# Optimization experiments

Hardware: AMD Instinct MI355X
Metric: run time of the kernel (lower is better)

The kernel has to match this reference:

```python
import jax, jax.numpy as jnp
import numpy as np

B, N, D_IN, D_OUT = 8, 256, 128, 128
EPS = 1e-5


def setup_inputs() -> dict:
    key = jax.random.key(0)
    ks = jax.random.split(key, 12)
    node_feats = jax.random.normal(ks[0], (B, N, D_IN), dtype=jnp.float32)
    adj_mask = jax.random.randint(ks[1], (B, N, N), 0, 2, dtype=jnp.int32)
    # ensure no fully-masked row (self-loop), matching typical adjacency
    adj_mask = adj_mask.at[:, jnp.arange(N), jnp.arange(N)].set(1)
    rel_positions = jax.random.normal(ks[2], (B, N, N, 2), dtype=jnp.float32)
    s_in = 1.0 / np.sqrt(D_IN)
    s_e = 1.0 / np.sqrt(2 * D_IN + 3)
    s_out = 1.0 / np.sqrt(D_OUT)
    return {
        "node_feats": node_feats,
        "adj_mask": adj_mask,
        "rel_positions": rel_positions,
        "Wn": jax.random.uniform(ks[3], (D_IN, D_OUT), jnp.float32, -s_in, s_in),
        "bn": jax.random.uniform(ks[4], (D_OUT,), jnp.float32, -s_in, s_in),
        "We1": jax.random.uniform(ks[5], (2 * D_IN + 3, D_OUT), jnp.float32, -s_e, s_e),
        "be1": jax.random.uniform(ks[6], (D_OUT,), jnp.float32, -s_e, s_e),
        "We2": jax.random.uniform(ks[7], (D_OUT, 1), jnp.float32, -s_out, s_out),
        "be2": jax.random.uniform(ks[8], (1,), jnp.float32, -s_out, s_out),
        "Wa": jax.random.uniform(ks[9], (D_OUT, D_OUT), jnp.float32, -s_out, s_out),
        "ba": jax.random.uniform(ks[10], (D_OUT,), jnp.float32, -s_out, s_out),
        "gamma": jnp.ones((D_OUT,), jnp.float32),
        "beta": jnp.zeros((D_OUT,), jnp.float32),
    }


def reference(node_feats, adj_mask, rel_positions, Wn, bn, We1, be1, We2, be2, Wa, ba, gamma, beta):
    D = node_feats.shape[-1]
    h = node_feats @ Wn + bn                                # (B,N,Dout)
    # Edge MLP first layer, factored to avoid the (B,N,N,2D+3) concat:
    # edge_input = [h_i, h_j, rel, dist]; Linear(edge_input) splits by rows of We1.
    a_i = node_feats @ We1[:D]                              # source-node part  (B,N,Dout)
    a_j = node_feats @ We1[D:2 * D]                         # target-node part  (B,N,Dout)
    rel_dist = jnp.linalg.norm(rel_positions, axis=-1, keepdims=True)  # (B,N,N,1)
    rel_feat = jnp.concatenate([rel_positions, rel_dist], axis=-1)     # (B,N,N,3)
    a_rel = rel_feat @ We1[2 * D:]                          # (B,N,N,Dout)
    hidden = jax.nn.relu(a_i[:, :, None, :] + a_j[:, None, :, :] + a_rel + be1)
    edge_scores = (hidden @ We2 + be2)[..., 0]              # (B,N,N)
    edge_scores = jnp.where(adj_mask == 0, -jnp.inf, edge_scores)
    w = jax.nn.softmax(edge_scores, axis=-1)
    w = jnp.where(jnp.isnan(w), 0.0, w)                     # fully-masked rows -> 0
    messages = jnp.einsum("bij,bjd->bid", w, h)             # (B,N,Dout)
    aggregated = jax.nn.relu(messages @ Wa + ba)            # dropout in eval mode -> identity
    x = node_feats + aggregated                             # D_IN == D_OUT -> residual
    mu = jnp.mean(x, axis=-1, keepdims=True)
    var = jnp.mean((x - mu) ** 2, axis=-1, keepdims=True)
    return (x - mu) / jnp.sqrt(var + EPS) * gamma + beta
```

## Files before the change

### kernel.cpp

```cpp
#include <hip/hip_runtime.h>
#include <math.h>

#define BB 8
#define NN 256
#define DD 128

#define PR 4
__global__ __launch_bounds__(256) void prep_kernel(
    const float* __restrict__ node, const float* __restrict__ Wn,
    const float* __restrict__ bn, const float* __restrict__ We1,
    const float* __restrict__ be1, float* __restrict__ h,
    float* __restrict__ ti, float* __restrict__ aj)
{
    __shared__ __align__(16) float sx[PR * DD];
    __shared__ float s_acc[12 * 128];
    int tid = threadIdx.x;
    int cp = tid & 63;
    int rp = (tid >> 6) & 1;
    int ks = tid >> 7;
    int row0 = blockIdx.x * PR;
    if (tid < 128) {
        int rr = tid >> 5, cc = (tid & 31) << 2;
        *(float4*)&sx[rr * DD + cc] = *(const float4*)&node[(size_t)(row0 + rr) * DD + cc];
    }
    __syncthreads();
    int d0 = cp << 1;
    int ra = rp << 1, rb = ra | 1;
    float ah[2] = {0.f, 0.f}, ai[2] = {0.f, 0.f}, ajc[2] = {0.f, 0.f};
    float bh[2] = {0.f, 0.f}, bi[2] = {0.f, 0.f}, bjc[2] = {0.f, 0.f};
    int k0 = ks << 6;
    for (int k = k0; k < k0 + 64; k += 4) {
        float4 xa = *(const float4*)&sx[ra * DD + k];
        float4 xb = *(const float4*)&sx[rb * DD + k];
        #pragma unroll
        for (int kk = 0; kk < 4; ++kk) {
            float2 w0 = *(const float2*)&Wn [(size_t)(k + kk) * DD + d0];
            float2 w1 = *(const float2*)&We1[(size_t)(k + kk) * DD + d0];
            float2 w2 = *(const float2*)&We1[(size_t)(DD + k + kk) * DD + d0];
            float xav = (kk == 0) ? xa.x : (kk == 1) ? xa.y : (kk == 2) ? xa.z : xa.w;
            float xbv = (kk == 0) ? xb.x : (kk == 1) ? xb.y : (kk == 2) ? xb.z : xb.w;
            ah[0] = fmaf(xav, w0.x, ah[0]); ah[1] = fmaf(xav, w0.y, ah[1]);
            ai[0] = fmaf(xav, w1.x, ai[0]); ai[1] = fmaf(xav, w1.y, ai[1]);
            ajc[0] = fmaf(xav, w2.x, ajc[0]); ajc[1] = fmaf(xav, w2.y, ajc[1]);
            bh[0] = fmaf(xbv, w0.x, bh[0]); bh[1] = fmaf(xbv, w0.y, bh[1]);
            bi[0] = fmaf(xbv, w1.x, bi[0]); bi[1] = fmaf(xbv, w1.y, bi[1]);
            bjc[0] = fmaf(xbv, w2.x, bjc[0]); bjc[1] = fmaf(xbv, w2.y, bjc[1]);
        }
    }
    int p = (rp << 6) | cp;
    if (ks == 1) {
        s_acc[0 * 128 + p] = ah[0];  s_acc[1 * 128 + p] = ah[1];
        s_acc[2 * 128 + p] = ai[0];  s_acc[3 * 128 + p] = ai[1];
        s_acc[4 * 128 + p] = ajc[0]; s_acc[5 * 128 + p] = ajc[1];
        s_acc[6 * 128 + p] = bh[0];  s_acc[7 * 128 + p] = bh[1];
        s_acc[8 * 128 + p] = bi[0];  s_acc[9 * 128 + p] = bi[1];
        s_acc[10 * 128 + p] = bjc[0]; s_acc[11 * 128 + p] = bjc[1];
    }
    __syncthreads();
    if (ks == 0) {
        float2 bn2  = *(const float2*)&bn[d0];
        float2 be12 = *(const float2*)&be1[d0];
        ah[0] += s_acc[0 * 128 + p] + bn2.x;  ah[1] += s_acc[1 * 128 + p] + bn2.y;
        ai[0] += s_acc[2 * 128 + p] + be12.x; ai[1] += s_acc[3 * 128 + p] + be12.y;
        ajc[0] += s_acc[4 * 128 + p];         ajc[1] += s_acc[5 * 128 + p];
        bh[0] += s_acc[6 * 128 + p] + bn2.x;  bh[1] += s_acc[7 * 128 + p] + bn2.y;
        bi[0] += s_acc[8 * 128 + p] + be12.x; bi[1] += s_acc[9 * 128 + p] + be12.y;
        bjc[0] += s_acc[10 * 128 + p];        bjc[1] += s_acc[11 * 128 + p];
        size_t oa = (size_t)(row0 + ra) * DD + d0;
        size_t ob = (size_t)(row0 + rb) * DD + d0;
        *(float2*)&h [oa] = make_float2(ah[0], ah[1]);
        *(float2*)&ti[oa] = make_float2(ai[0], ai[1]);
        *(float2*)&aj[oa] = make_float2(ajc[0], ajc[1]);
        *(float2*)&h [ob] = make_float2(bh[0], bh[1]);
        *(float2*)&ti[ob] = make_float2(bi[0], bi[1]);
        *(float2*)&aj[ob] = make_float2(bjc[0], bjc[1]);
    }
}

#define IT 4
__global__ __launch_bounds__(256, 2) void edge_kernel(
    const float* __restrict__ ti, const float* __restrict__ ajp,
    const float* __restrict__ rel, const int* __restrict__ adj,
    const float* __restrict__ We1, const float* __restrict__ We2,
    const float* __restrict__ be2, const float* __restrict__ h,
    const float* __restrict__ Wa, const float* __restrict__ ba,
    const float* __restrict__ node, const float* __restrict__ gamma,
    const float* __restrict__ beta, float* __restrict__ out)
{
    __shared__ __align__(16) float s_buf[NN * 32];
    __shared__ __align__(16) float s_w[NN * 4];
    __shared__ __align__(16) float s_m[DD * 4];
    __shared__ float s_red[IT][4];
    __shared__ float s_red2[IT][2][2];

    int tid = threadIdx.x;
    int b  = blockIdx.x >> 6;
    int i0 = (blockIdx.x & 63) << 2;
    int j = tid;

    const float2* rel2 = (const float2*)rel;
    float rx[IT], ry[IT], dsv[IT], sc[IT];
    int msk[IT];
    float be2v = be2[0];
    #pragma unroll
    for (int r = 0; r < IT; ++r) {
        float2 rp = rel2[(size_t)(b * NN + i0 + r) * NN + j];
        rx[r] = rp.x; ry[r] = rp.y;
        dsv[r] = sqrtf(rp.x * rp.x + rp.y * rp.y);
        msk[r] = adj[(size_t)(b * NN + i0 + r) * NN + j];
        sc[r] = be2v;
    }
    const float* TI = ti + (size_t)(b * NN + i0) * DD;
    const float* W0 = We1 + (size_t)(2 * DD + 0) * DD;
    const float* W1 = We1 + (size_t)(2 * DD + 1) * DD;
    const float* W2 = We1 + (size_t)(2 * DD + 2) * DD;
    const float* AJb = ajp + (size_t)b * NN * DD;

    for (int dc = 0; dc < DD; dc += 32) {
        __syncthreads();
        #pragma unroll
        for (int it = 0; it < 8; ++it) {
            int idx = tid + it * 256;
            int rr = idx >> 3, g = idx & 7;
            float4 v = *(const float4*)&AJb[(size_t)rr * DD + dc + (g << 2)];
            *(float4*)&s_buf[rr * 32 + ((g ^ (rr & 7)) << 2)] = v;
        }
        __syncthreads();
        #pragma unroll
        for (int g = 0; g < 8; ++g) {
            float4 a = *(const float4*)&s_buf[j * 32 + ((g ^ (j & 7)) << 2)];
            int dd = dc + (g << 2);
            float4 w0 = *(const float4*)&W0[dd];
            float4 w1 = *(const float4*)&W1[dd];
            float4 w2 = *(const float4*)&W2[dd];
            float4 e2 = *(const float4*)&We2[dd];
            #pragma unroll
            for (int r = 0; r < IT; ++r) {
                float4 t = *(const float4*)&TI[r * DD + dd];
                float v;
                v = fmaf(rx[r], w0.x, t.x + a.x); v = fmaf(ry[r], w1.x, v); v = fmaf(dsv[r], w2.x, v);
                sc[r] = fmaf(fmaxf(v, 0.f), e2.x, sc[r]);
                v = fmaf(rx[r], w0.y, t.y + a.y); v = fmaf(ry[r], w1.y, v); v = fmaf(dsv[r], w2.y, v);
                sc[r] = fmaf(fmaxf(v, 0.f), e2.y, sc[r]);
                v = fmaf(rx[r], w0.z, t.z + a.z); v = fmaf(ry[r], w1.z, v); v = fmaf(dsv[r], w2.z, v);
                sc[r] = fmaf(fmaxf(v, 0.f), e2.z, sc[r]);
                v = fmaf(rx[r], w0.w, t.w + a.w); v = fmaf(ry[r], w1.w, v); v = fmaf(dsv[r], w2.w, v);
                sc[r] = fmaf(fmaxf(v, 0.f), e2.w, sc[r]);
            }
        }
    }
    #pragma unroll
    for (int r = 0; r < IT; ++r) if (msk[r] == 0) sc[r] = -3.0e38f;

    int wave = tid >> 6, lane = tid & 63;
    float e[IT];
    {
        float m[IT];
        #pragma unroll
        for (int r = 0; r < IT; ++r) m[r] = sc[r];
        for (int off = 32; off > 0; off >>= 1) {
            #pragma unroll
            for (int r = 0; r < IT; ++r) m[r] = fmaxf(m[r], __shfl_xor(m[r], off));
        }
        if (lane == 0) {
            #pragma unroll
            for (int r = 0; r < IT; ++r) s_red[r][wave] = m[r];
        }
    }
    __syncthreads();
    #pragma unroll
    for (int r = 0; r < IT; ++r) {
        float M = fmaxf(fmaxf(s_red[r][0], s_red[r][1]), fmaxf(s_red[r][2], s_red[r][3]));
        e[r] = (msk[r] == 0) ? 0.f : __expf(sc[r] - M);
    }
    __syncthreads();
    {
        float s[IT];
        #pragma unroll
        for (int r = 0; r < IT; ++r) s[r] = e[r];
        for (int off = 32; off > 0; off >>= 1) {
            #pragma unroll
            for (int r = 0; r < IT; ++r) s[r] += __shfl_xor(s[r], off);
        }
        if (lane == 0) {
            #pragma unroll
            for (int r = 0; r < IT; ++r) s_red[r][wave] = s[r];
        }
    }
    __syncthreads();
    {
        float4 wq;
        float S0 = s_red[0][0] + s_red[0][1] + s_red[0][2] + s_red[0][3];
        float S1 = s_red[1][0] + s_red[1][1] + s_red[1][2] + s_red[1][3];
        float S2 = s_red[2][0] + s_red[2][1] + s_red[2][2] + s_red[2][3];
        float S3 = s_red[3][0] + s_red[3][1] + s_red[3][2] + s_red[3][3];
        wq.x = e[0] * __builtin_amdgcn_rcpf(S0);
        wq.y = e[1] * __builtin_amdgcn_rcpf(S1);
        wq.z = e[2] * __builtin_amdgcn_rcpf(S2);
        wq.w = e[3] * __builtin_amdgcn_rcpf(S3);
        *(float4*)&s_w[j << 2] = wq;
    }
    __syncthreads();

    float* s_part = s_buf;
    int g3 = tid & 31, sl = tid >> 5;
    {
        const float* hb = h + (size_t)b * NN * DD;
        float4 acc[IT];
        #pragma unroll
        for (int r = 0; r < IT; ++r) acc[r] = make_float4(0.f, 0.f, 0.f, 0.f);
        for (int q = 0; q < 32; ++q) {
            int jj = (sl << 5) + q;
            float4 hv = *(const float4*)&hb[(size_t)jj * DD + (g3 << 2)];
            float4 wv = *(const float4*)&s_w[jj << 2];
            acc[0].x = fmaf(wv.x, hv.x, acc[0].x); acc[0].y = fmaf(wv.x, hv.y, acc[0].y);
            acc[0].z = fmaf(wv.x, hv.z, acc[0].z); acc[0].w = fmaf(wv.x, hv.w, acc[0].w);
            acc[1].x = fmaf(wv.y, hv.x, acc[1].x); acc[1].y = fmaf(wv.y, hv.y, acc[1].y);
            acc[1].z = fmaf(wv.y, hv.z, acc[1].z); acc[1].w = fmaf(wv.y, hv.w, acc[1].w);
            acc[2].x = fmaf(wv.z, hv.x, acc[2].x); acc[2].y = fmaf(wv.z, hv.y, acc[2].y);
            acc[2].z = fmaf(wv.z, hv.z, acc[2].z); acc[2].w = fmaf(wv.z, hv.w, acc[2].w);
            acc[3].x = fmaf(wv.w, hv.x, acc[3].x); acc[3].y = fmaf(wv.w, hv.y, acc[3].y);
            acc[3].z = fmaf(wv.w, hv.z, acc[3].z); acc[3].w = fmaf(wv.w, hv.w, acc[3].w);
        }
        int base = ((sl << 5) + g3) * 20;
        #pragma unroll
        for (int r = 0; r < IT; ++r) *(float4*)&s_part[base + (r << 2)] = acc[r];
    }
    __syncthreads();
    #pragma unroll
    for (int p = 0; p < 2; ++p) {
        int o = tid + (p << 8);
        int r = o >> 7, d = o & 127;
        float s = 0.f;
        #pragma unroll
        for (int s2 = 0; s2 < 8; ++s2)
            s += s_part[((s2 << 5) + (d >> 2)) * 20 + (r << 2) + (d & 3)];
        s_m[(d << 2) + r] = s;
    }
    __syncthreads();

    {
        float4 ac[IT];
        #pragma unroll
        for (int r = 0; r < IT; ++r) ac[r] = make_float4(0.f, 0.f, 0.f, 0.f);
        for (int q = 0; q < 16; ++q) {
            int k = (sl << 4) + q;
            float4 wa = *(const float4*)&Wa[(size_t)k * DD + (g3 << 2)];
            float4 mv = *(const float4*)&s_m[k << 2];
            ac[0].x = fmaf(mv.x, wa.x, ac[0].x); ac[0].y = fmaf(mv.x, wa.y, ac[0].y);
            ac[0].z = fmaf(mv.x, wa.z, ac[0].z); ac[0].w = fmaf(mv.x, wa.w, ac[0].w);
            ac[1].x = fmaf(mv.y, wa.x, ac[1].x); ac[1].y = fmaf(mv.y, wa.y, ac[1].y);
            ac[1].z = fmaf(mv.y, wa.z, ac[1].z); ac[1].w = fmaf(mv.y, wa.w, ac[1].w);
            ac[2].x = fmaf(mv.z, wa.x, ac[2].x); ac[2].y = fmaf(mv.z, wa.y, ac[2].y);
            ac[2].z = fmaf(mv.z, wa.z, ac[2].z); ac[2].w = fmaf(mv.z, wa.w, ac[2].w);
            ac[3].x = fmaf(mv.w, wa.x, ac[3].x); ac[3].y = fmaf(mv.w, wa.y, ac[3].y);
            ac[3].z = fmaf(mv.w, wa.z, ac[3].z); ac[3].w = fmaf(mv.w, wa.w, ac[3].w);
        }
        __syncthreads();
        int base = ((sl << 5) + g3) * 20;
        #pragma unroll
        for (int r = 0; r < IT; ++r) *(float4*)&s_part[base + (r << 2)] = ac[r];
    }
    __syncthreads();

    {
        int d = tid & 127;
        int wh = (tid >> 6) & 1;
        float bad = ba[d], gam = gamma[d], bet = beta[d];
        float xv[2];
        #pragma unroll
        for (int p = 0; p < 2; ++p) {
            int o = tid + (p << 8);
            int r = o >> 7;
            float agg = 0.f;
            #pragma unroll
            for (int s2 = 0; s2 < 8; ++s2)
                agg += s_part[((s2 << 5) + (d >> 2)) * 20 + (r << 2) + (d & 3)];
            float x = node[(size_t)(b * NN + i0 + r) * DD + d] + fmaxf(agg + bad, 0.f);
            xv[p] = x;
            float s1 = x, s2v = x * x;
            for (int off = 32; off > 0; off >>= 1) {
                s1 += __shfl_xor(s1, off);
                s2v += __shfl_xor(s2v, off);
            }
            if (lane == 0) { s_red2[r][wh][0] = s1; s_red2[r][wh][1] = s2v; }
        }
        __syncthreads();
        #pragma unroll
        for (int p = 0; p < 2; ++p) {
            int o = tid + (p << 8);
            int r = o >> 7;
            float t1 = s_red2[r][0][0] + s_red2[r][1][0];
            float t2 = s_red2[r][0][1] + s_red2[r][1][1];
            float mu  = t1 * (1.0f / DD);
            float var = t2 * (1.0f / DD) - mu * mu;
            float inv = rsqrtf(var + 1e-5f);
            out[(size_t)(b * NN + i0 + r) * DD + d] = (xv[p] - mu) * inv * gam + bet;
        }
    }
}

extern "C" void kernel_launch(void* const* d_in, const int* in_sizes, int n_in,
                              void* d_out, int out_size, void* d_ws, size_t ws_size,
                              hipStream_t stream) {
    const float* node = (const float*)d_in[0];
    const int*   adj  = (const int*)d_in[1];
    const float* rel  = (const float*)d_in[2];
    const float* Wn   = (const float*)d_in[3];
    const float* bn   = (const float*)d_in[4];
    const float* We1  = (const float*)d_in[5];
    const float* be1  = (const float*)d_in[6];
    const float* We2  = (const float*)d_in[7];
    const float* be2  = (const float*)d_in[8];
    const float* Wa   = (const float*)d_in[9];
    const float* ba   = (const float*)d_in[10];
    const float* gamma = (const float*)d_in[11];
    const float* beta  = (const float*)d_in[12];
    float* out = (float*)d_out;

    float* ws  = (float*)d_ws;
    const int ROWS = BB * NN * DD;
    float* h   = ws;
    float* ti  = ws + ROWS;
    float* aj  = ws + 2 * ROWS;

    prep_kernel<<<BB * NN / PR, 256, 0, stream>>>(node, Wn, bn, We1, be1, h, ti, aj);
    edge_kernel<<<BB * NN / IT, 256, 0, stream>>>(ti, aj, rel, adj, We1, We2, be2,
                                                  h, Wa, ba, node, gamma, beta, out);
}
```

Before: 117.1 us.

## Compute edge MLP hidden layer in packed fp16 with fdot2 accumulation

Stores the per-node edge MLP projections and the rel-position/We2 weights as fp16, then evaluates the edge hidden layer with packed half2 FMAs and relu, accumulating scores via fdot2 into fp32. This halves the shared-memory and global traffic per chunk (64 dims per tile instead of 32) and doubles ALU throughput on the dominant N^2*D loop. It risks accuracy loss from fp16 rounding in pre-activation sums before softmax.

```diff
diff --git a/kernel.cpp b/kernel.cpp
--- a/kernel.cpp
+++ b/kernel.cpp
@@ -4,13 +4,36 @@
 #define BB 8
 #define NN 256
 #define DD 128
+
+typedef _Float16 h2 __attribute__((ext_vector_type(2)));
+union U4 { uint4 u; float4 f; h2 h[8]; };
+
+static __device__ __forceinline__ h2 relu2(h2 v) {
+    h2 z = {(_Float16)0, (_Float16)0};
+#if __has_builtin(__builtin_elementwise_max)
+    return __builtin_elementwise_max(v, z);
+#else
+    v.x = v.x > z.x ? v.x : z.x;
+    v.y = v.y > z.y ? v.y : z.y;
+    return v;
+#endif
+}
+
+static __device__ __forceinline__ float dot2acc(h2 a, h2 b, float c) {
+#if __has_builtin(__builtin_amdgcn_fdot2)
+    return __builtin_amdgcn_fdot2(a, b, c, false);
+#else
+    return fmaf((float)a.x, (float)b.x, fmaf((float)a.y, (float)b.y, c));
+#endif
+}
 
 #define PR 4
 __global__ __launch_bounds__(256) void prep_kernel(
     const float* __restrict__ node, const float* __restrict__ Wn,
     const float* __restrict__ bn, const float* __restrict__ We1,
-    const float* __restrict__ be1, float* __restrict__ h,
-    float* __restrict__ ti, float* __restrict__ aj)
+    const float* __restrict__ be1, const float* __restrict__ We2,
+    float* __restrict__ h, _Float16* __restrict__ tih,
+    _Float16* __restrict__ ajh, _Float16* __restrict__ wth)
 {
     __shared__ __align__(16) float sx[PR * DD];
     __shared__ float s_acc[12 * 128];
@@ -22,6 +45,12 @@
     if (tid < 128) {
         int rr = tid >> 5, cc = (tid & 31) << 2;
         *(float4*)&sx[rr * DD + cc] = *(const float4*)&node[(size_t)(row0 + rr) * DD + cc];
+    }
+    if (blockIdx.x == 0 && tid < 128) {
+        wth[0 * 128 + tid] = (_Float16)We1[(size_t)(2 * DD + 0) * DD + tid];
+        wth[1 * 128 + tid] = (_Float16)We1[(size_t)(2 * DD + 1) * DD + tid];
+        wth[2 * 128 + tid] = (_Float16)We1[(size_t)(2 * DD + 2) * DD + tid];
+        wth[3 * 128 + tid] = (_Float16)We2[tid];
     }
     __syncthreads();
     int d0 = cp << 1;
@@ -68,24 +97,24 @@
         bjc[0] += s_acc[10 * 128 + p];        bjc[1] += s_acc[11 * 128 + p];
         size_t oa = (size_t)(row0 + ra) * DD + d0;
         size_t ob = (size_t)(row0 + rb) * DD + d0;
-        *(float2*)&h [oa] = make_float2(ah[0], ah[1]);
-        *(float2*)&ti[oa] = make_float2(ai[0], ai[1]);
-        *(float2*)&aj[oa] = make_float2(ajc[0], ajc[1]);
-        *(float2*)&h [ob] = make_float2(bh[0], bh[1]);
-        *(float2*)&ti[ob] = make_float2(bi[0], bi[1]);
-        *(float2*)&aj[ob] = make_float2(bjc[0], bjc[1]);
+        *(float2*)&h[oa] = make_float2(ah[0], ah[1]);
+        *(float2*)&h[ob] = make_float2(bh[0], bh[1]);
+        *(h2*)&tih[oa] = (h2){(_Float16)ai[0], (_Float16)ai[1]};
+        *(h2*)&tih[ob] = (h2){(_Float16)bi[0], (_Float16)bi[1]};
+        *(h2*)&ajh[oa] = (h2){(_Float16)ajc[0], (_Float16)ajc[1]};
+        *(h2*)&ajh[ob] = (h2){(_Float16)bjc[0], (_Float16)bjc[1]};
     }
 }
 
 #define IT 4
 __global__ __launch_bounds__(256, 2) void edge_kernel(
-    const float* __restrict__ ti, const float* __restrict__ ajp,
-    const float* __restrict__ rel, const int* __restrict__ adj,
-    const float* __restrict__ We1, const float* __restrict__ We2,
-    const float* __restrict__ be2, const float* __restrict__ h,
-    const float* __restrict__ Wa, const float* __restrict__ ba,
-    const float* __restrict__ node, const float* __restrict__ gamma,
-    const float* __restrict__ beta, float* __restrict__ out)
+    const _Float16* __restrict__ tih, const _Float16* __restrict__ ajh,
+    const _Float16* __restrict__ wth, const float* __restrict__ rel,
+    const int* __restrict__ adj, const float* __restrict__ be2,
+    const float* __restrict__ h, const float* __restrict__ Wa,
+    const float* __restrict__ ba, const float* __restrict__ node,
+    const float* __restrict__ gamma, const float* __restrict__ beta,
+    float* __restrict__ out)
 {
     __shared__ __align__(16) float s_buf[NN * 32];
     __shared__ __align__(16) float s_w[NN * 4];
@@ -99,53 +128,53 @@
     int j = tid;
 
     const float2* rel2 = (const float2*)rel;
-    float rx[IT], ry[IT], dsv[IT], sc[IT];
+    float sc[IT];
     int msk[IT];
+    h2 rxh[IT], ryh[IT], dsh[IT];
     float be2v = be2[0];
     #pragma unroll
     for (int r = 0; r < IT; ++r) {
         float2 rp = rel2[(size_t)(b * NN + i0 + r) * NN + j];
-        rx[r] = rp.x; ry[r] = rp.y;
-        dsv[r] = sqrtf(rp.x * rp.x + rp.y * rp.y);
+        float ds = sqrtf(rp.x * rp.x + rp.y * rp.y);
+        _Float16 xh = (_Float16)rp.x, yh = (_Float16)rp.y, dh = (_Float16)ds;
+        rxh[r] = (h2){xh, xh}; ryh[r] = (h2){yh, yh}; dsh[r] = (h2){dh, dh};
         msk[r] = adj[(size_t)(b * NN + i0 + r) * NN + j];
         sc[r] = be2v;
     }
-    const float* TI = ti + (size_t)(b * NN + i0) * DD;
-    const float* W0 = We1 + (size_t)(2 * DD + 0) * DD;
-    const float* W1 = We1 + (size_t)(2 * DD + 1) * DD;
-    const float* W2 = We1 + (size_t)(2 * DD + 2) * DD;
-    const float* AJb = ajp + (size_t)b * NN * DD;
-
-    for (int dc = 0; dc < DD; dc += 32) {
+    const _Float16* TIH = tih + (size_t)(b * NN + i0) * DD;
+    const _Float16* AJH = ajh + (size_t)b * NN * DD;
+
+    for (int dc = 0; dc < DD; dc += 64) {
         __syncthreads();
         #pragma unroll
         for (int it = 0; it < 8; ++it) {
             int idx = tid + it * 256;
             int rr = idx >> 3, g = idx & 7;
-            float4 v = *(const float4*)&AJb[(size_t)rr * DD + dc + (g << 2)];
+            float4 v = *(const float4*)&AJH[(size_t)rr * DD + dc + (g << 3)];
             *(float4*)&s_buf[rr * 32 + ((g ^ (rr & 7)) << 2)] = v;
         }
         __syncthreads();
         #pragma unroll
-        for (int g = 0; g < 8; ++g) {
-            float4 a = *(const float4*)&s_buf[j * 32 + ((g ^ (j & 7)) << 2)];
-            int dd = dc + (g << 2);
-            float4 w0 = *(const float4*)&W0[dd];
-            float4 w1 = *(const float4*)&W1[dd];
-            float4 w2 = *(const float4*)&W2[dd];
-            float4 e2 = *(const float4*)&We2[dd];
+        for (int gg = 0; gg < 8; ++gg) {
+            U4 a; a.f = *(const float4*)&s_buf[j * 32 + ((gg ^ (j & 7)) << 2)];
+            int dd = dc + (gg << 3);
+            U4 w0u, w1u, w2u, e2u;
+            w0u.u = *(const uint4*)&wth[0 * 128 + dd];
+            w1u.u = *(const uint4*)&wth[1 * 128 + dd];
+            w2u.u = *(const uint4*)&wth[2 * 128 + dd];
+            e2u.u = *(const uint4*)&wth[3 * 128 + dd];
             #pragma unroll
             for (int r = 0; r < IT; ++r) {
-                float4 t = *(const float4*)&TI[r * DD + dd];
-                float v;
-                v = fmaf(rx[r], w0.x, t.x + a.x); v = fmaf(ry[r], w1.x, v); v = fmaf(dsv[r], w2.x, v);
-                sc[r] = fmaf(fmaxf(v, 0.f), e2.x, sc[r]);
-                v = fmaf(rx[r], w0.y, t.y + a.y); v = fmaf(ry[r], w1.y, v); v = fmaf(dsv[r], w2.y, v);
-                sc[r] = fmaf(fmaxf(v, 0.f), e2.y, sc[r]);
-                v = fmaf(rx[r], w0.z, t.z + a.z); v = fmaf(ry[r], w1.z, v); v = fmaf(dsv[r], w2.z, v);
-                sc[r] = fmaf(fmaxf(v, 0.f), e2.z, sc[r]);
-                v = fmaf(rx[r], w0.w, t.w + a.w); v = fmaf(ry[r], w1.w, v); v = fmaf(dsv[r], w2.w, v);
-                sc[r] = fmaf(fmaxf(v, 0.f), e2.w, sc[r]);
+                U4 t; t.u = *(const uint4*)&TIH[r * DD + dd];
+                #pragma unroll
+                for (int u = 0; u < 4; ++u) {
+                    h2 v = t.h[u] + a.h[u];
+                    v = rxh[r] * w0u.h[u] + v;
+                    v = ryh[r] * w1u.h[u] + v;
+                    v = dsh[r] * w2u.h[u] + v;
+                    v = relu2(v);
+                    sc[r] = dot2acc(v, e2u.h[u], sc[r]);
+                }
             }
         }
     }
@@ -320,11 +349,13 @@
 
     float* ws  = (float*)d_ws;
     const int ROWS = BB * NN * DD;
-    float* h   = ws;
-    float* ti  = ws + ROWS;
-    float* aj  = ws + 2 * ROWS;
-
-    prep_kernel<<<BB * NN / PR, 256, 0, stream>>>(node, Wn, bn, We1, be1, h, ti, aj);
-    edge_kernel<<<BB * NN / IT, 256, 0, stream>>>(ti, aj, rel, adj, We1, We2, be2,
+    float* h        = ws;
+    _Float16* tih   = (_Float16*)(ws + ROWS);
+    _Float16* ajh   = tih + ROWS;
+    _Float16* wth   = ajh + ROWS;
+
+    prep_kernel<<<BB * NN / PR, 256, 0, stream>>>(node, Wn, bn, We1, be1, We2,
+                                                  h, tih, ajh, wth);
+    edge_kernel<<<BB * NN / IT, 256, 0, stream>>>(tih, ajh, wth, rel, adj, be2,
                                                   h, Wa, ba, node, gamma, beta, out);
 }
```

New measurement: 111.8 us. -4.5%, faster.
